# Kernel tuning notes

Measured on AMD Instinct MI355X. Metric: run time of the kernel, lower is better.

The kernel has to match this reference:

```python
import jax, jax.numpy as jnp
import numpy as np

B, C, H, W = 8, 512, 64, 64


def setup_inputs() -> dict:
    key = jax.random.key(0)
    ks = jax.random.split(key, 8)
    return {
        "query": jax.random.normal(ks[0], (B, C, H, W), jnp.float32),
        "key": jax.random.normal(ks[1], (B, C, H, W), jnp.float32),
        "value": jax.random.normal(ks[2], (B, C, H, W), jnp.float32),
        "w1": jax.random.normal(ks[3], (4 * C, C), jnp.float32) * 0.02,
        "b1": jax.random.normal(ks[4], (4 * C,), jnp.float32) * 0.02,
        "w2": jax.random.normal(ks[5], (C, 4 * C), jnp.float32) * 0.02,
        "b2": jax.random.normal(ks[6], (C,), jnp.float32) * 0.02,
        "gamma": jax.random.normal(ks[7], (1,), jnp.float32),
    }


def reference(query, key, value, w1, b1, w2, b2, gamma):
    b, c, h, w = query.shape
    scale = c ** (-0.5)
    # flatten spatial dims: tokens n = h*w, channels c
    q = query.reshape(b, c, -1)   # [B,C,N]
    k = key.reshape(b, c, -1)     # [B,C,N]
    v = value.reshape(b, c, -1)   # [B,C,N]
    # attn[b,n,m] = softmax_m(q_n . k_m * scale)
    attn = jax.nn.softmax(jnp.einsum('bcn,bcm->bnm', q, k) * scale, axis=-1)
    out = jnp.einsum('bnm,bcm->bcn', attn, v).reshape(b, c, h, w)
    # 1x1-conv FFN: C -> 4C -> C with ReLU
    hdn = jax.nn.relu(jnp.einsum('bchw,dc->bdhw', out, w1) + b1[None, :, None, None])
    ffn = jnp.einsum('bdhw,cd->bchw', hdn, w2) + b2[None, :, None, None]
    return ffn * gamma + query
```

## Files before the change

### kernel.cpp

```cpp
#include <hip/hip_runtime.h>
#include <hip/hip_bf16.h>
#include <stdint.h>

#define BB 8
#define CC 512
#define NN 4096
#define QB 64
#define KB 64
#define D4 2048
#define NT (NN / KB)
#define SPAD 80

typedef short bf8 __attribute__((ext_vector_type(8)));
typedef float f32x4 __attribute__((ext_vector_type(4)));

__device__ __forceinline__ uint16_t f2bf(float f) {
  uint32_t u = __builtin_bit_cast(uint32_t, f);
  u = (u + 0x7FFFu + ((u >> 16) & 1u)) >> 16;
  return (uint16_t)u;
}
__device__ __forceinline__ float bf2f(uint16_t u) {
  return __builtin_bit_cast(float, (uint32_t)u << 16);
}

__device__ __forceinline__ void gl_lds16(const void* g, void* l) {
  __builtin_amdgcn_global_load_lds((__attribute__((address_space(1))) void*)g,
                                   (__attribute__((address_space(3))) void*)l, 16, 0, 0);
}

__global__ __launch_bounds__(256) void transpose_cast_k(const float* __restrict__ src,
                                                        uint16_t* __restrict__ dst,
                                                        float scale) {
  __shared__ float tile[32][33];
  int b = blockIdx.z;
  int n0 = blockIdx.x * 32, c0 = blockIdx.y * 32;
  int tx = threadIdx.x & 31, ty = threadIdx.x >> 5;
  const float* s = src + ((size_t)b * CC + c0) * NN + n0;
#pragma unroll
  for (int i = 0; i < 4; i++) {
    int c = ty + i * 8;
    tile[tx][c] = s[(size_t)c * NN + tx];
  }
  __syncthreads();
  uint16_t* d = dst + ((size_t)b * NN + n0) * CC + c0;
#pragma unroll
  for (int i = 0; i < 4; i++) {
    int n = ty + i * 8;
    d[(size_t)n * CC + tx] = f2bf(tile[n][tx] * scale);
  }
}

__global__ __launch_bounds__(256) void cast_k(const float* __restrict__ in,
                                              uint16_t* __restrict__ out, int n) {
  int i = (blockIdx.x * 256 + threadIdx.x) * 4;
  if (i >= n) return;
  float4 v = *(const float4*)(in + i);
  ushort4 o;
  o.x = f2bf(v.x); o.y = f2bf(v.y); o.z = f2bf(v.z); o.w = f2bf(v.w);
  *(ushort4*)(out + i) = o;
}

__global__ __launch_bounds__(256) void vpack_k(const float* __restrict__ v,
                                               uint16_t* __restrict__ vp) {
  const int blk = blockIdx.x;
  const int w = blk & 7, mtb = blk >> 3;
  const int mt = mtb & (NT - 1), b = mtb >> 6;
  const int tid = threadIdx.x;
#pragma unroll
  for (int h = 0; h < 2; h++) {
    const int c = tid + h * 256;
    const int ks = c >> 8, rt = (c >> 6) & 3, l = c & 63;
    const int llo = l & 15, lhi = l >> 4;
    const float* src = v + ((size_t)b * CC + w * 64 + rt * 16 + llo) * NN + mt * 64 + ks * 32 + lhi * 8;
    const float4 f0 = *(const float4*)src;
    const float4 f1 = *(const float4*)(src + 4);
    ushort4 o0, o1;
    o0.x = f2bf(f0.x); o0.y = f2bf(f0.y); o0.z = f2bf(f0.z); o0.w = f2bf(f0.w);
    o1.x = f2bf(f1.x); o1.y = f2bf(f1.y); o1.z = f2bf(f1.z); o1.w = f2bf(f1.w);
    uint16_t* dst = vp + (size_t)blk * 4096 + ks * 2048 + rt * 512 + l * 8;
    *(ushort4*)dst = o0;
    *(ushort4*)(dst + 4) = o1;
  }
}

__global__ __launch_bounds__(512) __attribute__((amdgpu_waves_per_eu(2, 2))) void attn_ffn_k(
    const uint16_t* __restrict__ Kt, const uint16_t* __restrict__ Vp,
    const uint16_t* __restrict__ W1b, const uint16_t* __restrict__ W2b,
    const float* __restrict__ b1v_, const float* __restrict__ b2,
    const float* __restrict__ gma, const float* __restrict__ qry,
    float* __restrict__ out) {
  __shared__ __attribute__((aligned(16))) uint16_t Ks[2][KB][CC];
  __shared__ __attribute__((aligned(16))) uint16_t SP[3][QB][SPAD];
  __shared__ float rsc[3][QB];
  __shared__ float lst[QB];

  const int bid = blockIdx.x + gridDim.x * blockIdx.y;
  const int b = bid & 7;
  const int n0 = (bid >> 3) * QB;
  const int tid = threadIdx.x;
  const int lane = tid & 63, wid = tid >> 6;
  const int lhi = lane >> 4, llo = lane & 15;
  const int r7 = llo & 7;

  const int srt = wid >> 1;
  const int sct0 = (wid & 1) * 2;

#pragma unroll
  for (int j = 0; j < 8; j++) {
    const int r = wid * 8 + j;
    gl_lds16(Kt + ((size_t)b * NN + r) * CC + ((lane ^ (r & 7)) << 3), &Ks[0][r][0]);
  }

  const float qscale = 0.044194173824159216f;
  bf8 qf[16];
  {
    const int qn = n0 + srt * 16 + llo;
    const float* qb = qry + (size_t)b * CC * NN + qn;
#pragma unroll
    for (int kc = 0; kc < 16; kc++) {
      bf8 f;
#pragma unroll
      for (int e = 0; e < 8; e++) {
        const int c = kc * 32 + lhi * 8 + e;
        f[e] = (short)f2bf(qb[(size_t)c * NN] * qscale);
      }
      qf[kc] = f;
    }
  }

  const f32x4 vzero = {0.f, 0.f, 0.f, 0.f};
  f32x4 acc[4][4];
#pragma unroll
  for (int i = 0; i < 4; i++)
#pragma unroll
    for (int j = 0; j < 4; j++) acc[i][j] = vzero;

  const uint16_t* vpw = Vp + (size_t)b * ((size_t)NT * 8 * 4096) + wid * 4096 + lane * 8;
  const int srow = tid >> 3, sj = tid & 7;
  float m_run = -__builtin_inff(), l_run = 0.f;
  bf8 av[2][4];

  auto QK = [&](int kbuf, int sb) {
    const uint16_t* k0row = &Ks[kbuf][sct0 * 16 + llo][0];
    const uint16_t* k1row = &Ks[kbuf][sct0 * 16 + 16 + llo][0];
    f32x4 s0 = vzero, s1 = vzero;
#pragma unroll
    for (int kc = 0; kc < 16; kc++) {
      const int g = ((kc * 4 + lhi) ^ r7) << 3;
      bf8 bk0 = *(const bf8*)(k0row + g);
      bf8 bk1 = *(const bf8*)(k1row + g);
      s0 = __builtin_amdgcn_mfma_f32_16x16x32_bf16(qf[kc], bk0, s0, 0, 0, 0);
      s1 = __builtin_amdgcn_mfma_f32_16x16x32_bf16(qf[kc], bk1, s1, 0, 0, 0);
    }
    const int n = srt * 16 + lhi * 4;
#pragma unroll
    for (int r = 0; r < 4; r++) {
      SP[sb][n + r][sct0 * 16 + llo] = f2bf(s0[r]);
      SP[sb][n + r][sct0 * 16 + 16 + llo] = f2bf(s1[r]);
    }
  };

  auto SOFTMAX = [&](int sb, bool last) {
    const bf8 sv8 = *(const bf8*)&SP[sb][srow][sj * 8];
    float sv[8];
#pragma unroll
    for (int k2 = 0; k2 < 8; k2++) sv[k2] = bf2f((uint16_t)sv8[k2]);
    float mx = fmaxf(fmaxf(fmaxf(sv[0], sv[1]), fmaxf(sv[2], sv[3])),
                     fmaxf(fmaxf(sv[4], sv[5]), fmaxf(sv[6], sv[7])));
    mx = fmaxf(mx, __shfl_xor(mx, 1, 8));
    mx = fmaxf(mx, __shfl_xor(mx, 2, 8));
    mx = fmaxf(mx, __shfl_xor(mx, 4, 8));
    const float nm = fmaxf(m_run, mx);
    const float rs = __expf(m_run - nm);
    float p[8], psum = 0.f;
#pragma unroll
    for (int k2 = 0; k2 < 8; k2++) {
      p[k2] = __expf(sv[k2] - nm);
      psum += p[k2];
    }
    bf8 pk;
#pragma unroll
    for (int k2 = 0; k2 < 8; k2++) pk[k2] = (short)f2bf(p[k2]);
    *(bf8*)&SP[sb][srow][sj * 8] = pk;
    psum += __shfl_xor(psum, 1, 8);
    psum += __shfl_xor(psum, 2, 8);
    psum += __shfl_xor(psum, 4, 8);
    l_run = l_run * rs + psum;
    m_run = nm;
    if (sj == 0) {
      rsc[sb][srow] = rs;
      if (last) lst[srow] = l_run;
    }
  };

  auto PV = [&](int sb) {
    float rsn[4];
#pragma unroll
    for (int nt = 0; nt < 4; nt++) rsn[nt] = rsc[sb][nt * 16 + llo];
#pragma unroll
    for (int rt = 0; rt < 4; rt++)
#pragma unroll
      for (int nt = 0; nt < 4; nt++) acc[rt][nt] *= rsn[nt];
#pragma unroll
    for (int ks = 0; ks < 2; ks++) {
      bf8 bp[4];
#pragma unroll
      for (int nt = 0; nt < 4; nt++)
        bp[nt] = *(const bf8*)&SP[sb][nt * 16 + llo][(ks * 4 + lhi) * 8];
#pragma unroll
      for (int rt = 0; rt < 4; rt++)
#pragma unroll
        for (int nt = 0; nt < 4; nt++)
          acc[rt][nt] = __builtin_amdgcn_mfma_f32_16x16x32_bf16(av[ks][rt], bp[nt], acc[rt][nt], 0, 0, 0);
    }
  };

  auto VLOAD = [&](int t) {
    const uint16_t* vt = vpw + (size_t)t * 32768;
#pragma unroll
    for (int ks = 0; ks < 2; ks++)
#pragma unroll
      for (int rt = 0; rt < 4; rt++)
        av[ks][rt] = *(const bf8*)(vt + ks * 2048 + rt * 512);
  };

  auto KDMA = [&](int t, int buf) {
#pragma unroll
    for (int j = 0; j < 8; j++) {
      const int r = wid * 8 + j;
      gl_lds16(Kt + ((size_t)b * NN + t * KB + r) * CC + ((lane ^ (r & 7)) << 3),
               &Ks[buf][r][0]);
    }
  };

  asm volatile("s_waitcnt vmcnt(0)" ::: "memory");
  __builtin_amdgcn_s_barrier();

  KDMA(1, 1);
  __builtin_amdgcn_s_setprio(1);
  QK(0, 0);
  __builtin_amdgcn_s_setprio(0);
  asm volatile("s_waitcnt vmcnt(0) lgkmcnt(0)" ::: "memory");
  __builtin_amdgcn_s_barrier();

  KDMA(2, 0);
  SOFTMAX(0, false);
  __builtin_amdgcn_s_setprio(1);
  QK(1, 1);
  __builtin_amdgcn_s_setprio(0);
  asm volatile("s_waitcnt vmcnt(0) lgkmcnt(0)" ::: "memory");
  __builtin_amdgcn_s_barrier();

  int sb0 = 2, sb1 = 1, sb2 = 0;
  for (int t = 2; t < NT; t++) {
    VLOAD(t - 2);
    if (t + 1 < NT) KDMA(t + 1, (t + 1) & 1);
    SOFTMAX(sb1, false);
    __builtin_amdgcn_s_setprio(1);
    PV(sb2);
    QK(t & 1, sb0);
    __builtin_amdgcn_s_setprio(0);
    asm volatile("s_waitcnt vmcnt(0) lgkmcnt(0)" ::: "memory");
    __builtin_amdgcn_s_barrier();
    const int tb = sb2; sb2 = sb1; sb1 = sb0; sb0 = tb;
  }

  VLOAD(NT - 2);
  SOFTMAX(sb1, true);
  __builtin_amdgcn_s_setprio(1);
  PV(sb2);
  __builtin_amdgcn_s_setprio(0);
  asm volatile("s_waitcnt vmcnt(0) lgkmcnt(0)" ::: "memory");
  __builtin_amdgcn_s_barrier();
  { const int tb = sb2; sb2 = sb1; sb1 = sb0; sb0 = tb; }

  VLOAD(NT - 1);
  __builtin_amdgcn_s_setprio(1);
  PV(sb2);
  __builtin_amdgcn_s_setprio(0);

  __syncthreads();

  float invl[4];
#pragma unroll
  for (int nt = 0; nt < 4; nt++) invl[nt] = 1.0f / lst[nt * 16 + llo];

  uint16_t(*Old)[CC] = (uint16_t(*)[CC]) & Ks[0][0][0];
#pragma unroll
  for (int rt = 0; rt < 4; rt++)
#pragma unroll
    for (int nt = 0; nt < 4; nt++) {
      ushort4 o4;
      o4.x = f2bf(acc[rt][nt][0] * invl[nt]);
      o4.y = f2bf(acc[rt][nt][1] * invl[nt]);
      o4.z = f2bf(acc[rt][nt][2] * invl[nt]);
      o4.w = f2bf(acc[rt][nt][3] * invl[nt]);
      const int gch = wid * 8 + rt * 2 + (lhi >> 1);
      *(ushort4*)(&Old[nt * 16 + llo][0] + ((gch ^ r7) << 3) + ((lhi & 1) << 2)) = o4;
    }

  uint16_t(*Hs)[CC] = (uint16_t(*)[CC]) & Ks[1][0][0];
  f32x4 facc[4][4];
#pragma unroll
  for (int i = 0; i < 4; i++)
#pragma unroll
    for (int j = 0; j < 4; j++) facc[i][j] = vzero;
  const float g = gma[0];
  const uint16_t* orow[4];
  const uint16_t* hrow[4];
#pragma unroll
  for (int nt = 0; nt < 4; nt++) {
    orow[nt] = &Old[nt * 16 + llo][0];
    hrow[nt] = &Hs[nt * 16 + llo][0];
  }

  for (int qtr = 0; qtr < 4; qtr++) {
    const int dq0 = qtr * 512;
    f32x4 hacc[4][4];
#pragma unroll
    for (int i = 0; i < 4; i++)
#pragma unroll
      for (int j = 0; j < 4; j++) hacc[i][j] = vzero;
    __syncthreads();
    __builtin_amdgcn_s_setprio(1);
#pragma unroll 2
    for (int kc8 = 0; kc8 < 64; kc8 += 4) {
      bf8 bo[4], aw[4];
      const int gof = ((kc8 + lhi) ^ r7) << 3;
#pragma unroll
      for (int nt = 0; nt < 4; nt++) bo[nt] = *(const bf8*)(orow[nt] + gof);
#pragma unroll
      for (int dt = 0; dt < 4; dt++) {
        const int d = dq0 + wid * 64 + dt * 16 + llo;
        aw[dt] = *(const bf8*)(W1b + (size_t)d * CC + (kc8 + lhi) * 8);
      }
#pragma unroll
      for (int dt = 0; dt < 4; dt++)
#pragma unroll
        for (int nt = 0; nt < 4; nt++)
          hacc[dt][nt] = __builtin_amdgcn_mfma_f32_16x16x32_bf16(aw[dt], bo[nt], hacc[dt][nt], 0, 0, 0);
    }
    __builtin_amdgcn_s_setprio(0);
#pragma unroll
    for (int dt = 0; dt < 4; dt++) {
      const int dg = dq0 + wid * 64 + dt * 16 + lhi * 4;
      const float4 b1v = *(const float4*)(b1v_ + dg);
#pragma unroll
      for (int nt = 0; nt < 4; nt++) {
        ushort4 h4;
        h4.x = f2bf(fmaxf(hacc[dt][nt][0] + b1v.x, 0.f));
        h4.y = f2bf(fmaxf(hacc[dt][nt][1] + b1v.y, 0.f));
        h4.z = f2bf(fmaxf(hacc[dt][nt][2] + b1v.z, 0.f));
        h4.w = f2bf(fmaxf(hacc[dt][nt][3] + b1v.w, 0.f));
        const int gch = wid * 8 + dt * 2 + (lhi >> 1);
        *(ushort4*)(&Hs[nt * 16 + llo][0] + ((gch ^ r7) << 3) + ((lhi & 1) << 2)) = h4;
      }
    }
    __syncthreads();
    __builtin_amdgcn_s_setprio(1);
#pragma unroll 2
    for (int kd8 = 0; kd8 < 64; kd8 += 4) {
      bf8 ah[4], bw[4];
      const int gof = ((kd8 + lhi) ^ r7) << 3;
#pragma unroll
      for (int nt = 0; nt < 4; nt++) ah[nt] = *(const bf8*)(hrow[nt] + gof);
#pragma unroll
      for (int ct = 0; ct < 4; ct++) {
        const int c = wid * 64 + ct * 16 + llo;
        bw[ct] = *(const bf8*)(W2b + (size_t)c * D4 + dq0 + (kd8 + lhi) * 8);
      }
#pragma unroll
      for (int nt = 0; nt < 4; nt++)
#pragma unroll
        for (int ct = 0; ct < 4; ct++)
          facc[nt][ct] = __builtin_amdgcn_mfma_f32_16x16x32_bf16(ah[nt], bw[ct], facc[nt][ct], 0, 0, 0);
    }
    __builtin_amdgcn_s_setprio(0);
  }

#pragma unroll
  for (int nt = 0; nt < 4; nt++) {
    const int n = n0 + nt * 16 + lhi * 4;
#pragma unroll
    for (int ct = 0; ct < 4; ct++) {
      const int c = wid * 64 + ct * 16 + llo;
      const float b2c = b2[c];
      const size_t off = ((size_t)b * CC + c) * NN + n;
      const float4 q4 = *(const float4*)(qry + off);
      float4 o4;
      o4.x = (facc[nt][ct][0] + b2c) * g + q4.x;
      o4.y = (facc[nt][ct][1] + b2c) * g + q4.y;
      o4.z = (facc[nt][ct][2] + b2c) * g + q4.z;
      o4.w = (facc[nt][ct][3] + b2c) * g + q4.w;
      *(float4*)(out + off) = o4;
    }
  }
}

extern "C" void kernel_launch(void* const* d_in, const int* in_sizes, int n_in,
                              void* d_out, int out_size, void* d_ws, size_t ws_size,
                              hipStream_t stream) {
  const float* q = (const float*)d_in[0];
  const float* k = (const float*)d_in[1];
  const float* v = (const float*)d_in[2];
  const float* w1 = (const float*)d_in[3];
  const float* b1 = (const float*)d_in[4];
  const float* w2 = (const float*)d_in[5];
  const float* b2 = (const float*)d_in[6];
  const float* gm = (const float*)d_in[7];
  float* out = (float*)d_out;

  uint16_t* Kt = (uint16_t*)d_ws;
  uint16_t* Vp = Kt + (size_t)BB * NN * CC;
  uint16_t* W1b = Vp + (size_t)BB * NN * CC;
  uint16_t* W2b = W1b + (size_t)D4 * CC;

  dim3 tgrid(NN / 32, CC / 32, BB);
  transpose_cast_k<<<tgrid, 256, 0, stream>>>(k, Kt, 1.0f);
  vpack_k<<<BB * NT * 8, 256, 0, stream>>>(v, Vp);
  cast_k<<<(D4 * CC / 4 + 255) / 256, 256, 0, stream>>>(w1, W1b, D4 * CC);
  cast_k<<<(CC * D4 / 4 + 255) / 256, 256, 0, stream>>>(w2, W2b, CC * D4);
  attn_ffn_k<<<dim3(NN / QB, BB), 512, 0, stream>>>(Kt, Vp, W1b, W2b, b1, b2, gm, q, out);
}
```

Measured before the change: 688.3 us.

## Switch QK^T path to FP8 e4m3 MFMA with FP8 key staging

Keys are now transposed and cast to FP8 e4m3 instead of bf16, and Q fragments are packed as FP8. The QK score matmul uses the fp8 MFMA instruction, which halves key bytes loaded through LDS and global memory and uses the higher-rate fp8 path. Shared memory is reorganized into a single byte buffer with manual offsets, and the K DMA swizzle is adapted to 512-byte rows. FP8 quantization of Q and K lowers score precision and may affect accuracy against the fp32 reference.

```diff
diff --git a/kernel.cpp b/kernel.cpp
--- a/kernel.cpp
+++ b/kernel.cpp
@@ -1,5 +1,6 @@
 #include <hip/hip_runtime.h>
 #include <hip/hip_bf16.h>
+#include <hip/hip_fp8.h>
 #include <stdint.h>
 
 #define BB 8
@@ -13,6 +14,7 @@
 
 typedef short bf8 __attribute__((ext_vector_type(8)));
 typedef float f32x4 __attribute__((ext_vector_type(4)));
+typedef unsigned long long u64;
 
 __device__ __forceinline__ uint16_t f2bf(float f) {
   uint32_t u = __builtin_bit_cast(uint32_t, f);
@@ -22,15 +24,18 @@
 __device__ __forceinline__ float bf2f(uint16_t u) {
   return __builtin_bit_cast(float, (uint32_t)u << 16);
 }
+__device__ __forceinline__ uint8_t f2e4m3(float f) {
+  __hip_fp8_e4m3 t(f);
+  return (uint8_t)t.__x;
+}
 
 __device__ __forceinline__ void gl_lds16(const void* g, void* l) {
   __builtin_amdgcn_global_load_lds((__attribute__((address_space(1))) void*)g,
                                    (__attribute__((address_space(3))) void*)l, 16, 0, 0);
 }
 
-__global__ __launch_bounds__(256) void transpose_cast_k(const float* __restrict__ src,
-                                                        uint16_t* __restrict__ dst,
-                                                        float scale) {
+__global__ __launch_bounds__(256) void transpose_cast_fp8_k(const float* __restrict__ src,
+                                                            uint8_t* __restrict__ dst) {
   __shared__ float tile[32][33];
   int b = blockIdx.z;
   int n0 = blockIdx.x * 32, c0 = blockIdx.y * 32;
@@ -42,11 +47,11 @@
     tile[tx][c] = s[(size_t)c * NN + tx];
   }
   __syncthreads();
-  uint16_t* d = dst + ((size_t)b * NN + n0) * CC + c0;
+  uint8_t* d = dst + (((size_t)b * NN + n0) << 9) + c0;
 #pragma unroll
   for (int i = 0; i < 4; i++) {
     int n = ty + i * 8;
-    d[(size_t)n * CC + tx] = f2bf(tile[n][tx] * scale);
+    d[((size_t)n << 9) + tx] = f2e4m3(tile[n][tx]);
   }
 }
 
@@ -84,15 +89,16 @@
 }
 
 __global__ __launch_bounds__(512) __attribute__((amdgpu_waves_per_eu(2, 2))) void attn_ffn_k(
-    const uint16_t* __restrict__ Kt, const uint16_t* __restrict__ Vp,
+    const uint8_t* __restrict__ Ktf8, const uint16_t* __restrict__ Vp,
     const uint16_t* __restrict__ W1b, const uint16_t* __restrict__ W2b,
     const float* __restrict__ b1v_, const float* __restrict__ b2,
     const float* __restrict__ gma, const float* __restrict__ qry,
     float* __restrict__ out) {
-  __shared__ __attribute__((aligned(16))) uint16_t Ks[2][KB][CC];
-  __shared__ __attribute__((aligned(16))) uint16_t SP[3][QB][SPAD];
-  __shared__ float rsc[3][QB];
-  __shared__ float lst[QB];
+  __shared__ __attribute__((aligned(16))) uint8_t smem[131840];
+  uint8_t* KsP = smem;
+  uint16_t(*SP)[QB][SPAD] = (uint16_t(*)[QB][SPAD])(smem + 65536);
+  float* rscP = (float*)(smem + 96256);
+  float* lstP = (float*)(smem + 131072);
 
   const int bid = blockIdx.x + gridDim.x * blockIdx.y;
   const int b = bid & 7;
@@ -105,26 +111,33 @@
   const int srt = wid >> 1;
   const int sct0 = (wid & 1) * 2;
 
-#pragma unroll
-  for (int j = 0; j < 8; j++) {
-    const int r = wid * 8 + j;
-    gl_lds16(Kt + ((size_t)b * NN + r) * CC + ((lane ^ (r & 7)) << 3), &Ks[0][r][0]);
-  }
+  auto KDMA = [&](int t, int buf) {
+#pragma unroll
+    for (int j = 0; j < 4; j++) {
+      const int r0 = wid * 8 + j * 2;
+      const int rr = r0 + (lane >> 5);
+      const int ch = (lane & 31) ^ (rr & 7);
+      gl_lds16(Ktf8 + (((size_t)b * NN + (size_t)t * KB + rr) << 9) + (ch << 4),
+               KsP + buf * 32768 + r0 * 512);
+    }
+  };
+
+  KDMA(0, 0);
 
   const float qscale = 0.044194173824159216f;
-  bf8 qf[16];
+  u64 qf8[16];
   {
     const int qn = n0 + srt * 16 + llo;
     const float* qb = qry + (size_t)b * CC * NN + qn;
 #pragma unroll
     for (int kc = 0; kc < 16; kc++) {
-      bf8 f;
+      u64 v = 0;
 #pragma unroll
       for (int e = 0; e < 8; e++) {
         const int c = kc * 32 + lhi * 8 + e;
-        f[e] = (short)f2bf(qb[(size_t)c * NN] * qscale);
+        v |= (u64)f2e4m3(qb[(size_t)c * NN] * qscale) << (8 * e);
       }
-      qf[kc] = f;
+      qf8[kc] = v;
     }
   }
 
@@ -141,16 +154,17 @@
   bf8 av[2][4];
 
   auto QK = [&](int kbuf, int sb) {
-    const uint16_t* k0row = &Ks[kbuf][sct0 * 16 + llo][0];
-    const uint16_t* k1row = &Ks[kbuf][sct0 * 16 + 16 + llo][0];
+    const uint8_t* k0row = KsP + kbuf * 32768 + (sct0 * 16 + llo) * 512;
+    const uint8_t* k1row = k0row + 16 * 512;
     f32x4 s0 = vzero, s1 = vzero;
 #pragma unroll
     for (int kc = 0; kc < 16; kc++) {
-      const int g = ((kc * 4 + lhi) ^ r7) << 3;
-      bf8 bk0 = *(const bf8*)(k0row + g);
-      bf8 bk1 = *(const bf8*)(k1row + g);
-      s0 = __builtin_amdgcn_mfma_f32_16x16x32_bf16(qf[kc], bk0, s0, 0, 0, 0);
-      s1 = __builtin_amdgcn_mfma_f32_16x16x32_bf16(qf[kc], bk1, s1, 0, 0, 0);
+      const int g8 = kc * 4 + lhi;
+      const int off = (((g8 >> 1) ^ r7) << 4) + ((g8 & 1) << 3);
+      const long long bk0 = *(const long long*)(k0row + off);
+      const long long bk1 = *(const long long*)(k1row + off);
+      s0 = __builtin_amdgcn_mfma_f32_16x16x32_fp8_fp8((long long)qf8[kc], bk0, s0, 0, 0, 0);
+      s1 = __builtin_amdgcn_mfma_f32_16x16x32_fp8_fp8((long long)qf8[kc], bk1, s1, 0, 0, 0);
     }
     const int n = srt * 16 + lhi * 4;
 #pragma unroll
@@ -188,15 +202,15 @@
     l_run = l_run * rs + psum;
     m_run = nm;
     if (sj == 0) {
-      rsc[sb][srow] = rs;
-      if (last) lst[srow] = l_run;
+      rscP[sb * QB + srow] = rs;
+      if (last) lstP[srow] = l_run;
     }
   };
 
   auto PV = [&](int sb) {
     float rsn[4];
 #pragma unroll
-    for (int nt = 0; nt < 4; nt++) rsn[nt] = rsc[sb][nt * 16 + llo];
+    for (int nt = 0; nt < 4; nt++) rsn[nt] = rscP[sb * QB + nt * 16 + llo];
 #pragma unroll
     for (int rt = 0; rt < 4; rt++)
 #pragma unroll
@@ -222,15 +236,6 @@
 #pragma unroll
       for (int rt = 0; rt < 4; rt++)
         av[ks][rt] = *(const bf8*)(vt + ks * 2048 + rt * 512);
-  };
-
-  auto KDMA = [&](int t, int buf) {
-#pragma unroll
-    for (int j = 0; j < 8; j++) {
-      const int r = wid * 8 + j;
-      gl_lds16(Kt + ((size_t)b * NN + t * KB + r) * CC + ((lane ^ (r & 7)) << 3),
-               &Ks[buf][r][0]);
-    }
   };
 
   asm volatile("s_waitcnt vmcnt(0)" ::: "memory");
@@ -283,9 +288,9 @@
 
   float invl[4];
 #pragma unroll
-  for (int nt = 0; nt < 4; nt++) invl[nt] = 1.0f / lst[nt * 16 + llo];
-
-  uint16_t(*Old)[CC] = (uint16_t(*)[CC]) & Ks[0][0][0];
+  for (int nt = 0; nt < 4; nt++) invl[nt] = 1.0f / lstP[nt * 16 + llo];
+
+  uint16_t(*Old)[CC] = (uint16_t(*)[CC])smem;
 #pragma unroll
   for (int rt = 0; rt < 4; rt++)
 #pragma unroll
@@ -299,7 +304,7 @@
       *(ushort4*)(&Old[nt * 16 + llo][0] + ((gch ^ r7) << 3) + ((lhi & 1) << 2)) = o4;
     }
 
-  uint16_t(*Hs)[CC] = (uint16_t(*)[CC]) & Ks[1][0][0];
+  uint16_t(*Hs)[CC] = (uint16_t(*)[CC])(smem + 65536);
   f32x4 facc[4][4];
 #pragma unroll
   for (int i = 0; i < 4; i++)
@@ -410,15 +415,15 @@
   const float* gm = (const float*)d_in[7];
   float* out = (float*)d_out;
 
-  uint16_t* Kt = (uint16_t*)d_ws;
-  uint16_t* Vp = Kt + (size_t)BB * NN * CC;
+  uint8_t* Ktf8 = (uint8_t*)d_ws;
+  uint16_t* Vp = (uint16_t*)(Ktf8 + (size_t)BB * NN * 512);
   uint16_t* W1b = Vp + (size_t)BB * NN * CC;
   uint16_t* W2b = W1b + (size_t)D4 * CC;
 
   dim3 tgrid(NN / 32, CC / 32, BB);
-  transpose_cast_k<<<tgrid, 256, 0, stream>>>(k, Kt, 1.0f);
+  transpose_cast_fp8_k<<<tgrid, 256, 0, stream>>>(k, Ktf8);
   vpack_k<<<BB * NT * 8, 256, 0, stream>>>(v, Vp);
   cast_k<<<(D4 * CC / 4 + 255) / 256, 256, 0, stream>>>(w1, W1b, D4 * CC);
   cast_k<<<(CC * D4 / 4 + 255) / 256, 256, 0, stream>>>(w2, W2b, CC * D4);
-  attn_ffn_k<<<dim3(NN / QB, BB), 512, 0, stream>>>(Kt, Vp, W1b, W2b, b1, b2, gm, q, out);
-}
+  attn_ffn_k<<<dim3(NN / QB, BB), 512, 0, stream>>>(Ktf8, Vp, W1b, W2b, b1, b2, gm, q, out);
+}
```

New measurement: 637.7 us. -7.4%, faster.
